# Performance work log

Measured on AMD Instinct MI355X. Metric: run time of the kernel, lower is better.

The kernel has to match this reference:

```python
import jax, jax.numpy as jnp
import numpy as np

V, E, H, Z, T = 8185, 353, 191, 13, 25
START = 19


def _lstm(x, h, c, k, rk, b):
    # Keras LSTMCell: gates ordered i, f, g(candidate), o
    gates = x @ k + h @ rk + b                      # (B, 4H)
    i, f, g, o = jnp.split(gates, 4, axis=-1)
    c_new = jax.nn.sigmoid(f) * c + jax.nn.sigmoid(i) * jnp.tanh(g)
    h_new = jax.nn.sigmoid(o) * jnp.tanh(c_new)
    return h_new, c_new


def setup_inputs() -> dict:
    key = jax.random.key(0)
    ks = jax.random.split(key, 18)
    B = 256
    s = 0.05
    inp = {
        "inputs": jax.random.randint(ks[0], (B, T), 0, V),
        "epsilon": jax.random.normal(ks[1], (Z,), jnp.float32),
        "emb": jax.random.normal(ks[2], (V, E), jnp.float32) * s,
        "inf_k": jax.random.normal(ks[3], (E, 4 * H), jnp.float32) * s,
        "inf_rk": jax.random.normal(ks[4], (H, 4 * H), jnp.float32) * s,
        "inf_b": jnp.zeros((4 * H,), jnp.float32),
        "mu_w": jax.random.normal(ks[5], (H, Z), jnp.float32) * s,
        "mu_b": jnp.zeros((Z,), jnp.float32),
        "sig_w": jax.random.normal(ks[6], (H, Z), jnp.float32) * s,
        "sig_b": jnp.zeros((Z,), jnp.float32),
        "init_w": jax.random.normal(ks[7], (Z, H), jnp.float32) * s,
        "init_b": jnp.zeros((H,), jnp.float32),
        "gen_k": jax.random.normal(ks[8], (E, 4 * H), jnp.float32) * s,
        "gen_rk": jax.random.normal(ks[9], (H, 4 * H), jnp.float32) * s,
        "gen_b": jnp.zeros((4 * H,), jnp.float32),
        "out_w": jax.random.normal(ks[10], (H, V), jnp.float32) * s,
        "out_b": jnp.zeros((V,), jnp.float32),
    }
    return inp


def reference(inputs, epsilon, emb, inf_k, inf_rk, inf_b, mu_w, mu_b,
              sig_w, sig_b, init_w, init_b, gen_k, gen_rk, gen_b,
              out_w, out_b):
    B = inputs.shape[0]
    # ----- encoder (inference LSTM over the full sequence) -----
    inf_emb = emb[inputs]                             # (B, T, E)

    def enc_step(carry, x_t):
        h, c = carry
        h, c = _lstm(x_t, h, c, inf_k, inf_rk, inf_b)
        return (h, c), None

    h0 = jnp.zeros((B, H), emb.dtype)
    (h_enc, _), _ = jax.lax.scan(enc_step, (h0, h0),
                                 jnp.swapaxes(inf_emb, 0, 1))  # scan over T

    mu = h_enc @ mu_w + mu_b                          # (B, Z)
    sigma = h_enc @ sig_w + sig_b                     # (B, Z)
    z = mu + epsilon * sigma                          # shared epsilon (Z,)

    init_state = z @ init_w + init_b                  # (B, H)
    emb0 = jnp.broadcast_to(emb[START], (B, E))       # start token embedding

    def dec_step(carry, _):
        h, c, x = carry
        h, c = _lstm(x, h, c, gen_k, gen_rk, gen_b)
        logits = h @ out_w + out_b                    # (B, V)
        new_ind = jnp.argmax(logits, axis=-1)         # (B,)
        x_next = emb[new_ind]                         # (B, E)
        return (h, c, x_next), logits

    _, logits_seq = jax.lax.scan(dec_step, (init_state, init_state, emb0),
                                 None, length=T)      # (T, B, V)
    return jnp.swapaxes(logits_seq, 0, 1)             # (B, T, V)
```

## Files before the change

### kernel.cpp

```cpp
#include <hip/hip_runtime.h>
#include <math.h>

#define V_  8185
#define E_  353
#define H_  191
#define FH_ 764
#define Z_  13
#define T_  25
#define START_ 19
#define VP_ 8192
#define NTL 64
#define RKS 192

__device__ __forceinline__ float sigf(float x) { return 1.0f / (1.0f + expf(-x)); }

__global__ __launch_bounds__(256) void prep_w(const float* __restrict__ ow,
                                              const float* __restrict__ rkA,
                                              const float* __restrict__ rkB,
                                              float* __restrict__ WP,
                                              float* __restrict__ rkT) {
  int i = blockIdx.x * 256 + threadIdx.x;
  if (i < H_ * VP_) {
    int k = i >> 13;
    int j = i & (VP_ - 1);
    WP[i] = (j < V_) ? ow[(size_t)k * V_ + j] : 0.0f;
  } else {
    int i2 = i - H_ * VP_;
    if (i2 < 2 * FH_ * RKS) {
      int w = i2 / (FH_ * RKS), rem = i2 - w * (FH_ * RKS);
      int col4 = rem / RKS, k = rem - col4 * RKS;
      const float* src = w ? rkB : rkA;
      rkT[i2] = (k < H_) ? src[(size_t)k * FH_ + col4] : 0.0f;
    }
  }
}

__global__ __launch_bounds__(256) void gemm_ew(const float* __restrict__ emb,
                                               const float* __restrict__ W,
                                               float* __restrict__ C, int M,
                                               const int* __restrict__ inputs,
                                               int mode, int B) {
  __shared__ __align__(16) float AT[E_ * 16];
  const int tid = threadIdx.x;
  const int n0 = blockIdx.x * 256;
  const int m0 = blockIdx.y * 16;
  for (int i = tid; i < 16 * E_; i += 256) {
    int r = i / E_, k = i - r * E_;
    int m = m0 + r;
    float v = 0.0f;
    if (m < M) {
      int row;
      if (mode == 0) row = m;
      else { int t = m / B, b = m - t * B; row = inputs[b * T_ + t]; }
      v = emb[(size_t)row * E_ + k];
    }
    AT[k * 16 + r] = v;
  }
  __syncthreads();
  const int lane = tid & 63;
  const int w4 = (tid >> 6) * 4;
  const int j = n0 + lane * 4;
  if (j >= FH_) return;
  float4 c0 = {0,0,0,0}, c1 = {0,0,0,0}, c2 = {0,0,0,0}, c3 = {0,0,0,0};
  const float* wc = W + j;
  const float* at = AT + w4;
  for (int k = 0; k < E_; ++k) {
    float4 wv = *(const float4*)(wc + (size_t)k * FH_);
    float4 a  = *(const float4*)(at + k * 16);
    c0.x = fmaf(a.x, wv.x, c0.x); c0.y = fmaf(a.x, wv.y, c0.y);
    c0.z = fmaf(a.x, wv.z, c0.z); c0.w = fmaf(a.x, wv.w, c0.w);
    c1.x = fmaf(a.y, wv.x, c1.x); c1.y = fmaf(a.y, wv.y, c1.y);
    c1.z = fmaf(a.y, wv.z, c1.z); c1.w = fmaf(a.y, wv.w, c1.w);
    c2.x = fmaf(a.z, wv.x, c2.x); c2.y = fmaf(a.z, wv.y, c2.y);
    c2.z = fmaf(a.z, wv.z, c2.z); c2.w = fmaf(a.z, wv.w, c2.w);
    c3.x = fmaf(a.w, wv.x, c3.x); c3.y = fmaf(a.w, wv.y, c3.y);
    c3.z = fmaf(a.w, wv.z, c3.z); c3.w = fmaf(a.w, wv.w, c3.w);
  }
  const int mb = m0 + w4;
  if (mb + 0 < M) *(float4*)(C + (size_t)(mb + 0) * FH_ + j) = c0;
  if (mb + 1 < M) *(float4*)(C + (size_t)(mb + 1) * FH_ + j) = c1;
  if (mb + 2 < M) *(float4*)(C + (size_t)(mb + 2) * FH_ + j) = c2;
  if (mb + 3 < M) *(float4*)(C + (size_t)(mb + 3) * FH_ + j) = c3;
}

__global__ __launch_bounds__(256) void lstm_step(const float* __restrict__ xk,
                                                 const float* __restrict__ rkT,
                                                 const float* __restrict__ bias,
                                                 const float* __restrict__ h_in,
                                                 const float* __restrict__ c_in,
                                                 float* __restrict__ h_out,
                                                 float* __restrict__ c_out,
                                                 const float* __restrict__ pmax,
                                                 const int* __restrict__ pidx,
                                                 int mode, int first) {
  __shared__ float rks[32][193];
  __shared__ __align__(16) float hs[8][RKS];
  __shared__ float xs[8 * 32];
  __shared__ float bs[32];
  __shared__ int   tk[8];
  __shared__ float pv[8 * NTL];
  __shared__ int   pi[8 * NTL];
  __shared__ float cbv[8][4];
  __shared__ int   cbi[8][4];
  __shared__ float gb[32 * 8];

  const int tid = threadIdx.x;
  const int c0 = blockIdx.x * 8;
  const int m0 = blockIdx.y * 8;

  if (mode) {
    if (first) {
      if (tid < 8) tk[tid] = START_;
    } else {
      for (int i = tid; i < 8 * NTL; i += 256) {
        int row = i >> 6, s = i & (NTL - 1);
        pv[i] = pmax[(size_t)(m0 + row) * NTL + s];
        pi[i] = pidx[(size_t)(m0 + row) * NTL + s];
      }
      __syncthreads();
      if (tid < 32) {
        int row = tid >> 2, cch = tid & 3;
        int base = row * NTL + cch * 16;
        float bv = pv[base]; int bi = pi[base];
        for (int s = 1; s < 16; ++s) {
          float v = pv[base + s]; int ii = pi[base + s];
          if (v > bv || (v == bv && ii < bi)) { bv = v; bi = ii; }
        }
        cbv[row][cch] = bv; cbi[row][cch] = bi;
      }
      __syncthreads();
      if (tid < 8) {
        float bv = cbv[tid][0]; int bi = cbi[tid][0];
        for (int cch = 1; cch < 4; ++cch) {
          float v = cbv[tid][cch]; int ii = cbi[tid][cch];
          if (v > bv || (v == bv && ii < bi)) { bv = v; bi = ii; }
        }
        tk[tid] = bi;
      }
    }
    __syncthreads();
  }

  for (int i = tid; i < 32 * 48; i += 256) {
    int qq = i / 48, kq = (i - qq * 48) * 4;
    int jj2 = c0 + (qq & 7), g = qq >> 3;
    float4 v = {0, 0, 0, 0};
    if (jj2 < H_) v = *(const float4*)(rkT + (size_t)(jj2 + H_ * g) * RKS + kq);
    rks[qq][kq]     = v.x; rks[qq][kq + 1] = v.y;
    rks[qq][kq + 2] = v.z; rks[qq][kq + 3] = v.w;
  }
  for (int i = tid; i < 8 * H_; i += 256) {
    int r = i / H_, k = i - r * H_;
    hs[r][k] = h_in[(size_t)m0 * H_ + i];
  }
  {
    int i = tid;
    int row = i >> 5, q = i & 31;
    int jj = c0 + (q & 7);
    int jg = jj + H_ * (q >> 3);
    float xv = 0.0f;
    if (jj < H_) {
      const float* xrow = mode ? (xk + (size_t)tk[row] * FH_)
                               : (xk + (size_t)(m0 + row) * FH_);
      xv = xrow[jg];
    }
    xs[i] = xv;
  }
  if (tid < 32) {
    int jj = c0 + (tid & 7);
    bs[tid] = (jj < H_) ? bias[jj + H_ * (tid >> 3)] : 0.0f;
  }
  __syncthreads();

  const int q = tid & 31, rg = tid >> 5;
  const int jj = c0 + (q & 7);
  float a0 = 0.0f;
  if (jj < H_) {
    const float* rr = rks[q];
    const float* hp = hs[rg];
    int k = 0;
    for (; k < 188; k += 4) {
      float4 hv = *(const float4*)(hp + k);
      a0 = fmaf(hv.x, rr[k    ], a0);
      a0 = fmaf(hv.y, rr[k + 1], a0);
      a0 = fmaf(hv.z, rr[k + 2], a0);
      a0 = fmaf(hv.w, rr[k + 3], a0);
    }
    for (; k < H_; ++k) a0 = fmaf(hp[k], rr[k], a0);
  }
  gb[q * 8 + rg] = a0;
  __syncthreads();

  if (tid < 64) {
    int cc = tid & 7, row = tid >> 3;
    int jc = c0 + cc;
    if (jc < H_) {
      float gi = gb[(cc     ) * 8 + row] + xs[row * 32 + cc     ] + bs[cc];
      float gf = gb[( 8 + cc) * 8 + row] + xs[row * 32 +  8 + cc] + bs[ 8 + cc];
      float gg = gb[(16 + cc) * 8 + row] + xs[row * 32 + 16 + cc] + bs[16 + cc];
      float go = gb[(24 + cc) * 8 + row] + xs[row * 32 + 24 + cc] + bs[24 + cc];
      float co = c_in[(size_t)(m0 + row) * H_ + jc];
      float cn = sigf(gf) * co + sigf(gi) * tanhf(gg);
      float hn = sigf(go) * tanhf(cn);
      c_out[(size_t)(m0 + row) * H_ + jc] = cn;
      h_out[(size_t)(m0 + row) * H_ + jc] = hn;
    }
  }
}

__global__ __launch_bounds__(256) void logits_argmax(const float* __restrict__ h,
                                                     const float* __restrict__ wp,
                                                     const float* __restrict__ ob,
                                                     float* __restrict__ out, int t,
                                                     float* __restrict__ pmax,
                                                     int* __restrict__ pidx) {
  __shared__ __align__(16) float AT[H_ * 20];
  const int tid = threadIdx.x;
  const int n0 = blockIdx.x * 128;
  const int m0 = blockIdx.y * 16;
  for (int i = tid; i < 16 * H_; i += 256) {
    int r = i / H_, k = i - r * H_;
    AT[k * 20 + r] = h[(size_t)m0 * H_ + i];
  }
  __syncthreads();

  const int cq = tid & 31;
  const int ro = tid >> 5;
  const int j = n0 + cq * 4;
  const float* wc = wp + j;
  const float* at = AT + ro * 2;
  float4 acc0 = {0,0,0,0}, acc1 = {0,0,0,0};

#define LFMA(AK, WV) { \
    float2 a_ = *(const float2*)(at + (AK) * 20); \
    acc0.x = fmaf(a_.x, WV.x, acc0.x); acc0.y = fmaf(a_.x, WV.y, acc0.y); \
    acc0.z = fmaf(a_.x, WV.z, acc0.z); acc0.w = fmaf(a_.x, WV.w, acc0.w); \
    acc1.x = fmaf(a_.y, WV.x, acc1.x); acc1.y = fmaf(a_.y, WV.y, acc1.y); \
    acc1.z = fmaf(a_.y, WV.z, acc1.z); acc1.w = fmaf(a_.y, WV.w, acc1.w); }

  float4 w0 = *(const float4*)(wc);
  int k = 0;
  for (; k < 190; k += 2) {
    float4 w1 = *(const float4*)(wc + (size_t)(k + 1) * VP_);
    LFMA(k, w0)
    w0 = *(const float4*)(wc + (size_t)(k + 2) * VP_);
    LFMA(k + 1, w1)
  }
  LFMA(190, w0)
#undef LFMA

  float bias4[4];
#pragma unroll
  for (int u = 0; u < 4; ++u) bias4[u] = (j + u < V_) ? ob[j + u] : 0.0f;
  const bool tile_full = (n0 + 128 <= V_);
#pragma unroll
  for (int rr = 0; rr < 2; ++rr) {
    const int b = m0 + ro * 2 + rr;
    float4 acc = rr ? acc1 : acc0;
    float v[4] = {acc.x + bias4[0], acc.y + bias4[1],
                  acc.z + bias4[2], acc.w + bias4[3]};
    float* orow = out + ((size_t)b * T_ + t) * V_ + j;
    if (tile_full) {
      orow[0] = v[0]; orow[1] = v[1]; orow[2] = v[2]; orow[3] = v[3];
    } else {
#pragma unroll
      for (int u = 0; u < 4; ++u)
        if (j + u < V_) orow[u] = v[u];
    }
    float bv = -INFINITY; int bi = 0;
#pragma unroll
    for (int u = 0; u < 4; ++u)
      if (j + u < V_ && v[u] > bv) { bv = v[u]; bi = j + u; }
#pragma unroll
    for (int off = 1; off < 32; off <<= 1) {
      float ov = __shfl_xor(bv, off, 64);
      int   oi = __shfl_xor(bi, off, 64);
      if (ov > bv || (ov == bv && oi < bi)) { bv = ov; bi = oi; }
    }
    if ((tid & 31) == 0) {
      pmax[(size_t)b * NTL + blockIdx.x] = bv;
      pidx[(size_t)b * NTL + blockIdx.x] = bi;
    }
  }
}

__global__ __launch_bounds__(64) void latent_k(const float* __restrict__ h,
                                               const float* __restrict__ eps,
                                               const float* __restrict__ mu_w,
                                               const float* __restrict__ mu_b,
                                               const float* __restrict__ sig_w,
                                               const float* __restrict__ sig_b,
                                               const float* __restrict__ iw,
                                               const float* __restrict__ ib,
                                               float* __restrict__ h0,
                                               float* __restrict__ c0) {
  __shared__ float zs[4 * Z_];
  const int tid = threadIdx.x;
  const int m0 = blockIdx.x * 4;
  if (tid < 4 * Z_) {
    int row = tid / Z_, qz = tid - row * Z_;
    const float* hr = h + (size_t)(m0 + row) * H_;
    float mu = mu_b[qz], sg = sig_b[qz];
    for (int k = 0; k < H_; ++k) {
      float hv = hr[k];
      mu = fmaf(hv, mu_w[k * Z_ + qz], mu);
      sg = fmaf(hv, sig_w[k * Z_ + qz], sg);
    }
    zs[tid] = mu + eps[qz] * sg;
  }
  __syncthreads();
  for (int i = tid; i < 4 * H_; i += 64) {
    int row = i / H_, col = i - row * H_;
    float acc = ib[col];
#pragma unroll
    for (int qz = 0; qz < Z_; ++qz)
      acc = fmaf(zs[row * Z_ + qz], iw[qz * H_ + col], acc);
    h0[(size_t)(m0 + row) * H_ + col] = acc;
    c0[(size_t)(m0 + row) * H_ + col] = acc;
  }
}

extern "C" void kernel_launch(void* const* d_in, const int* in_sizes, int n_in,
                              void* d_out, int out_size, void* d_ws, size_t ws_size,
                              hipStream_t stream) {
  const int*   inputs = (const int*)  d_in[0];
  const float* eps    = (const float*)d_in[1];
  const float* emb    = (const float*)d_in[2];
  const float* inf_k  = (const float*)d_in[3];
  const float* inf_rk = (const float*)d_in[4];
  const float* inf_b  = (const float*)d_in[5];
  const float* mu_w   = (const float*)d_in[6];
  const float* mu_b   = (const float*)d_in[7];
  const float* sig_w  = (const float*)d_in[8];
  const float* sig_b  = (const float*)d_in[9];
  const float* init_w = (const float*)d_in[10];
  const float* init_b = (const float*)d_in[11];
  const float* gen_k  = (const float*)d_in[12];
  const float* gen_rk = (const float*)d_in[13];
  const float* gen_b  = (const float*)d_in[14];
  const float* out_w  = (const float*)d_in[15];
  const float* out_b  = (const float*)d_in[16];
  float* out = (float*)d_out;

  const int B = in_sizes[0] / T_;
  const int BH = B * H_;

  float* ws = (float*)d_ws;
  size_t off = 0;
  float* EK = ws + off; off += (size_t)V_ * FH_;
  float* XK = ws + off; off += (size_t)T_ * B * FH_;
  float* WP = ws + off; off += (size_t)H_ * VP_;
  float* rkT = ws + off; off += (size_t)2 * FH_ * RKS;
  float* hbase = ws + off; off += (size_t)8 * BH;
  float* he[2] = {hbase + 0 * BH, hbase + 2 * BH};
  float* ce[2] = {hbase + 1 * BH, hbase + 3 * BH};
  float* hd[2] = {hbase + 4 * BH, hbase + 6 * BH};
  float* cd[2] = {hbase + 5 * BH, hbase + 7 * BH};
  float* pmax = ws + off; off += (size_t)B * NTL;
  int*   pidx = (int*)(ws + off); off += (size_t)B * NTL;
  float* rkT_inf = rkT;
  float* rkT_gen = rkT + (size_t)FH_ * RKS;

  hipMemsetAsync(hbase, 0, (size_t)2 * BH * sizeof(float), stream);

  prep_w<<<(H_ * VP_ + 2 * FH_ * RKS + 255) / 256, 256, 0, stream>>>(
      out_w, inf_rk, gen_rk, WP, rkT);
  gemm_ew<<<dim3(3, (V_ + 15) / 16), 256, 0, stream>>>(emb, gen_k, EK, V_, nullptr, 0, B);
  gemm_ew<<<dim3(3, (T_ * B) / 16), 256, 0, stream>>>(emb, inf_k, XK, T_ * B, inputs, 1, B);

  for (int t = 0; t < T_; ++t) {
    lstm_step<<<dim3(24, B / 8), 256, 0, stream>>>(
        XK + (size_t)t * B * FH_, rkT_inf, inf_b,
        he[t & 1], ce[t & 1], he[(t + 1) & 1], ce[(t + 1) & 1],
        nullptr, nullptr, 0, 0);
  }

  latent_k<<<B / 4, 64, 0, stream>>>(he[T_ & 1], eps, mu_w, mu_b, sig_w, sig_b,
                                     init_w, init_b, hd[0], cd[0]);

  for (int t = 0; t < T_; ++t) {
    lstm_step<<<dim3(24, B / 8), 256, 0, stream>>>(
        EK, rkT_gen, gen_b,
        hd[t & 1], cd[t & 1], hd[(t + 1) & 1], cd[(t + 1) & 1],
        pmax, pidx, 1, (t == 0) ? 1 : 0);
    logits_argmax<<<dim3(NTL, B / 16), 256, 0, stream>>>(
        hd[(t + 1) & 1], WP, out_b, out, t, pmax, pidx);
  }
}
```

Before: 1.726 ms.

## Fuse encoder LSTM time loop and latent projection into one per-row kernel

```diff
diff --git a/kernel.cpp b/kernel.cpp
--- a/kernel.cpp
+++ b/kernel.cpp
@@ -15,7 +15,6 @@
 __device__ __forceinline__ float sigf(float x) { return 1.0f / (1.0f + expf(-x)); }
 
 __global__ __launch_bounds__(256) void prep_w(const float* __restrict__ ow,
-                                              const float* __restrict__ rkA,
                                               const float* __restrict__ rkB,
                                               float* __restrict__ WP,
                                               float* __restrict__ rkT) {
@@ -26,11 +25,9 @@
     WP[i] = (j < V_) ? ow[(size_t)k * V_ + j] : 0.0f;
   } else {
     int i2 = i - H_ * VP_;
-    if (i2 < 2 * FH_ * RKS) {
-      int w = i2 / (FH_ * RKS), rem = i2 - w * (FH_ * RKS);
-      int col4 = rem / RKS, k = rem - col4 * RKS;
-      const float* src = w ? rkB : rkA;
-      rkT[i2] = (k < H_) ? src[(size_t)k * FH_ + col4] : 0.0f;
+    if (i2 < FH_ * RKS) {
+      int col4 = i2 / RKS, k = i2 - col4 * RKS;
+      rkT[i2] = (k < H_) ? rkB[(size_t)k * FH_ + col4] : 0.0f;
     }
   }
 }
@@ -83,6 +80,77 @@
   if (mb + 3 < M) *(float4*)(C + (size_t)(mb + 3) * FH_ + j) = c3;
 }
 
+__global__ __launch_bounds__(256) void encoder_row(
+    const float* __restrict__ xk,
+    const float* __restrict__ rk,
+    const float* __restrict__ bias,
+    const float* __restrict__ eps,
+    const float* __restrict__ mu_w, const float* __restrict__ mu_b,
+    const float* __restrict__ sig_w, const float* __restrict__ sig_b,
+    const float* __restrict__ iw, const float* __restrict__ ib,
+    float* __restrict__ h0o, float* __restrict__ c0o, int B) {
+  __shared__ float h[H_ + 1];
+  __shared__ float gd[FH_];
+  __shared__ float zs[Z_];
+  const int tid = threadIdx.x;
+  const int b = blockIdx.x;
+  const bool dotT = (tid < H_);
+  const int col = tid * 4;
+
+  float4 b4 = {0, 0, 0, 0};
+  if (dotT) b4 = *(const float4*)(bias + col);
+  float creg = 0.0f;
+  if (tid < H_) h[tid] = 0.0f;
+  __syncthreads();
+
+  for (int t = 0; t < T_; ++t) {
+    if (dotT) {
+      float4 a = {0, 0, 0, 0};
+      const float* rp = rk + col;
+#pragma unroll 4
+      for (int k = 0; k < H_; ++k) {
+        float hk = h[k];
+        float4 w = *(const float4*)(rp + (size_t)k * FH_);
+        a.x = fmaf(hk, w.x, a.x); a.y = fmaf(hk, w.y, a.y);
+        a.z = fmaf(hk, w.z, a.z); a.w = fmaf(hk, w.w, a.w);
+      }
+      float4 x4 = *(const float4*)(xk + ((size_t)t * B + b) * FH_ + col);
+      gd[col + 0] = (a.x + x4.x) + b4.x;
+      gd[col + 1] = (a.y + x4.y) + b4.y;
+      gd[col + 2] = (a.z + x4.z) + b4.z;
+      gd[col + 3] = (a.w + x4.w) + b4.w;
+    }
+    __syncthreads();
+    if (tid < H_) {
+      float gi = gd[tid], gf = gd[H_ + tid];
+      float gg = gd[2 * H_ + tid], go = gd[3 * H_ + tid];
+      float cn = sigf(gf) * creg + sigf(gi) * tanhf(gg);
+      creg = cn;
+      h[tid] = sigf(go) * tanhf(cn);
+    }
+    __syncthreads();
+  }
+
+  if (tid < Z_) {
+    float mu = mu_b[tid], sg = sig_b[tid];
+    for (int k = 0; k < H_; ++k) {
+      float hv = h[k];
+      mu = fmaf(hv, mu_w[k * Z_ + tid], mu);
+      sg = fmaf(hv, sig_w[k * Z_ + tid], sg);
+    }
+    zs[tid] = mu + eps[tid] * sg;
+  }
+  __syncthreads();
+  if (tid < H_) {
+    float acc = ib[tid];
+#pragma unroll
+    for (int z = 0; z < Z_; ++z)
+      acc = fmaf(zs[z], iw[z * H_ + tid], acc);
+    h0o[(size_t)b * H_ + tid] = acc;
+    c0o[(size_t)b * H_ + tid] = acc;
+  }
+}
+
 __global__ __launch_bounds__(256) void lstm_step(const float* __restrict__ xk,
                                                  const float* __restrict__ rkT,
                                                  const float* __restrict__ bias,
@@ -92,7 +160,7 @@
                                                  float* __restrict__ c_out,
                                                  const float* __restrict__ pmax,
                                                  const int* __restrict__ pidx,
-                                                 int mode, int first) {
+                                                 int first) {
   __shared__ float rks[32][193];
   __shared__ __align__(16) float hs[8][RKS];
   __shared__ float xs[8 * 32];
@@ -108,38 +176,36 @@
   const int c0 = blockIdx.x * 8;
   const int m0 = blockIdx.y * 8;
 
-  if (mode) {
-    if (first) {
-      if (tid < 8) tk[tid] = START_;
-    } else {
-      for (int i = tid; i < 8 * NTL; i += 256) {
-        int row = i >> 6, s = i & (NTL - 1);
-        pv[i] = pmax[(size_t)(m0 + row) * NTL + s];
-        pi[i] = pidx[(size_t)(m0 + row) * NTL + s];
+  if (first) {
+    if (tid < 8) tk[tid] = START_;
+  } else {
+    for (int i = tid; i < 8 * NTL; i += 256) {
+      int row = i >> 6, s = i & (NTL - 1);
+      pv[i] = pmax[(size_t)(m0 + row) * NTL + s];
+      pi[i] = pidx[(size_t)(m0 + row) * NTL + s];
+    }
+    __syncthreads();
+    if (tid < 32) {
+      int row = tid >> 2, cch = tid & 3;
+      int base = row * NTL + cch * 16;
+      float bv = pv[base]; int bi = pi[base];
+      for (int s = 1; s < 16; ++s) {
+        float v = pv[base + s]; int ii = pi[base + s];
+        if (v > bv || (v == bv && ii < bi)) { bv = v; bi = ii; }
       }
-      __syncthreads();
-      if (tid < 32) {
-        int row = tid >> 2, cch = tid & 3;
-        int base = row * NTL + cch * 16;
-        float bv = pv[base]; int bi = pi[base];
-        for (int s = 1; s < 16; ++s) {
-          float v = pv[base + s]; int ii = pi[base + s];
-          if (v > bv || (v == bv && ii < bi)) { bv = v; bi = ii; }
-        }
-        cbv[row][cch] = bv; cbi[row][cch] = bi;
+      cbv[row][cch] = bv; cbi[row][cch] = bi;
+    }
+    __syncthreads();
+    if (tid < 8) {
+      float bv = cbv[tid][0]; int bi = cbi[tid][0];
+      for (int cch = 1; cch < 4; ++cch) {
+        float v = cbv[tid][cch]; int ii = cbi[tid][cch];
+        if (v > bv || (v == bv && ii < bi)) { bv = v; bi = ii; }
       }
-      __syncthreads();
-      if (tid < 8) {
-        float bv = cbv[tid][0]; int bi = cbi[tid][0];
-        for (int cch = 1; cch < 4; ++cch) {
-          float v = cbv[tid][cch]; int ii = cbi[tid][cch];
-          if (v > bv || (v == bv && ii < bi)) { bv = v; bi = ii; }
-        }
-        tk[tid] = bi;
-      }
-    }
-    __syncthreads();
-  }
+      tk[tid] = bi;
+    }
+  }
+  __syncthreads();
 
   for (int i = tid; i < 32 * 48; i += 256) {
     int qq = i / 48, kq = (i - qq * 48) * 4;
@@ -159,11 +225,7 @@
     int jj = c0 + (q & 7);
     int jg = jj + H_ * (q >> 3);
     float xv = 0.0f;
-    if (jj < H_) {
-      const float* xrow = mode ? (xk + (size_t)tk[row] * FH_)
-                               : (xk + (size_t)(m0 + row) * FH_);
-      xv = xrow[jg];
-    }
+    if (jj < H_) xv = xk[(size_t)tk[row] * FH_ + jg];
     xs[i] = xv;
   }
   if (tid < 32) {
@@ -281,42 +343,6 @@
       pmax[(size_t)b * NTL + blockIdx.x] = bv;
       pidx[(size_t)b * NTL + blockIdx.x] = bi;
     }
-  }
-}
-
-__global__ __launch_bounds__(64) void latent_k(const float* __restrict__ h,
-                                               const float* __restrict__ eps,
-                                               const float* __restrict__ mu_w,
-                                               const float* __restrict__ mu_b,
-                                               const float* __restrict__ sig_w,
-                                               const float* __restrict__ sig_b,
-                                               const float* __restrict__ iw,
-                                               const float* __restrict__ ib,
-                                               float* __restrict__ h0,
-                                               float* __restrict__ c0) {
-  __shared__ float zs[4 * Z_];
-  const int tid = threadIdx.x;
-  const int m0 = blockIdx.x * 4;
-  if (tid < 4 * Z_) {
-    int row = tid / Z_, qz = tid - row * Z_;
-    const float* hr = h + (size_t)(m0 + row) * H_;
-    float mu = mu_b[qz], sg = sig_b[qz];
-    for (int k = 0; k < H_; ++k) {
-      float hv = hr[k];
-      mu = fmaf(hv, mu_w[k * Z_ + qz], mu);
-      sg = fmaf(hv, sig_w[k * Z_ + qz], sg);
-    }
-    zs[tid] = mu + eps[qz] * sg;
-  }
-  __syncthreads();
-  for (int i = tid; i < 4 * H_; i += 64) {
-    int row = i / H_, col = i - row * H_;
-    float acc = ib[col];
-#pragma unroll
-    for (int qz = 0; qz < Z_; ++qz)
-      acc = fmaf(zs[row * Z_ + qz], iw[qz * H_ + col], acc);
-    h0[(size_t)(m0 + row) * H_ + col] = acc;
-    c0[(size_t)(m0 + row) * H_ + col] = acc;
   }
 }
 
@@ -350,39 +376,27 @@
   float* EK = ws + off; off += (size_t)V_ * FH_;
   float* XK = ws + off; off += (size_t)T_ * B * FH_;
   float* WP = ws + off; off += (size_t)H_ * VP_;
-  float* rkT = ws + off; off += (size_t)2 * FH_ * RKS;
-  float* hbase = ws + off; off += (size_t)8 * BH;
-  float* he[2] = {hbase + 0 * BH, hbase + 2 * BH};
-  float* ce[2] = {hbase + 1 * BH, hbase + 3 * BH};
-  float* hd[2] = {hbase + 4 * BH, hbase + 6 * BH};
-  float* cd[2] = {hbase + 5 * BH, hbase + 7 * BH};
+  float* rkT_gen = ws + off; off += (size_t)FH_ * RKS;
+  float* hbase = ws + off; off += (size_t)4 * BH;
+  float* hd[2] = {hbase + 0 * BH, hbase + 2 * BH};
+  float* cd[2] = {hbase + 1 * BH, hbase + 3 * BH};
   float* pmax = ws + off; off += (size_t)B * NTL;
   int*   pidx = (int*)(ws + off); off += (size_t)B * NTL;
-  float* rkT_inf = rkT;
-  float* rkT_gen = rkT + (size_t)FH_ * RKS;
-
-  hipMemsetAsync(hbase, 0, (size_t)2 * BH * sizeof(float), stream);
-
-  prep_w<<<(H_ * VP_ + 2 * FH_ * RKS + 255) / 256, 256, 0, stream>>>(
-      out_w, inf_rk, gen_rk, WP, rkT);
+
+  prep_w<<<(H_ * VP_ + FH_ * RKS + 255) / 256, 256, 0, stream>>>(
+      out_w, gen_rk, WP, rkT_gen);
   gemm_ew<<<dim3(3, (V_ + 15) / 16), 256, 0, stream>>>(emb, gen_k, EK, V_, nullptr, 0, B);
   gemm_ew<<<dim3(3, (T_ * B) / 16), 256, 0, stream>>>(emb, inf_k, XK, T_ * B, inputs, 1, B);
 
-  for (int t = 0; t < T_; ++t) {
-    lstm_step<<<dim3(24, B / 8), 256, 0, stream>>>(
-        XK + (size_t)t * B * FH_, rkT_inf, inf_b,
-        he[t & 1], ce[t & 1], he[(t + 1) & 1], ce[(t + 1) & 1],
-        nullptr, nullptr, 0, 0);
-  }
-
-  latent_k<<<B / 4, 64, 0, stream>>>(he[T_ & 1], eps, mu_w, mu_b, sig_w, sig_b,
-                                     init_w, init_b, hd[0], cd[0]);
+  encoder_row<<<B, 256, 0, stream>>>(XK, inf_rk, inf_b, eps,
+                                     mu_w, mu_b, sig_w, sig_b,
+                                     init_w, init_b, hd[0], cd[0], B);
 
   for (int t = 0; t < T_; ++t) {
     lstm_step<<<dim3(24, B / 8), 256, 0, stream>>>(
         EK, rkT_gen, gen_b,
         hd[t & 1], cd[t & 1], hd[(t + 1) & 1], cd[(t + 1) & 1],
-        pmax, pidx, 1, (t == 0) ? 1 : 0);
+        pmax, pidx, (t == 0) ? 1 : 0);
     logits_argmax<<<dim3(NTL, B / 16), 256, 0, stream>>>(
         hd[(t + 1) & 1], WP, out_b, out, t, pmax, pidx);
   }
```

Result: slower. 1.831 ms (+6.1%).
